# Optimization experiments

Hardware: AMD Instinct MI355X
Metric: run time of the kernel (lower is better)

Reference implementation:

```python
import jax, jax.numpy as jnp
import numpy as np

N, E, D, H, C, L = 100000, 1280000, 64, 4, 16, 3  # nodes, edges, dim, heads, head_dim, layers
NEG_SLOPE = 0.2
LN_EPS = 1e-5


def setup_inputs() -> dict:
    key = jax.random.key(0)
    ks = jax.random.split(key, 6)
    scale = 1.0 / np.sqrt(D)
    x = jax.random.normal(ks[0], (N, D), dtype=jnp.float32)
    edge_index = jax.random.randint(ks[1], (2, E), 0, N, dtype=jnp.int64)
    Wl = jax.random.normal(ks[2], (L, D, H * C), dtype=jnp.float32) * scale  # lin_l (source)
    Wr = jax.random.normal(ks[3], (L, D, H * C), dtype=jnp.float32) * scale  # lin_r (target)
    att = jax.random.normal(ks[4], (L, H, C), dtype=jnp.float32) * scale
    bias = jnp.zeros((L, H * C), dtype=jnp.float32)
    gamma = jnp.ones((L, D), dtype=jnp.float32)
    beta = jnp.zeros((L, D), dtype=jnp.float32)
    return dict(x=x, edge_index=edge_index, Wl=Wl, Wr=Wr, att=att, bias=bias, gamma=gamma, beta=beta)


def _gatv2_conv(x, src, dst, Wl, Wr, att, bias):
    # GATv2Conv (concat=True, share_weights=False, negative_slope=0.2)
    n = x.shape[0]
    xl = (x @ Wl).reshape(n, H, C)  # messages from source nodes
    xr = (x @ Wr).reshape(n, H, C)  # target-side transform
    m = xl[src] + xr[dst]  # [E', H, C]
    e = jnp.einsum('ehc,hc->eh', jax.nn.leaky_relu(m, NEG_SLOPE), att)  # [E', H]
    emax = jax.ops.segment_max(e, dst, num_segments=n)
    p = jnp.exp(e - emax[dst])
    denom = jax.ops.segment_sum(p, dst, num_segments=n)
    alpha = p / denom[dst]  # self-loops guarantee denom > 0
    out = jax.ops.segment_sum(alpha[:, :, None] * xl[src], dst, num_segments=n)  # [N, H, C]
    return out.reshape(n, H * C) + bias


def _layernorm(x, gamma, beta):
    mu = jnp.mean(x, axis=-1, keepdims=True)
    var = jnp.mean(jnp.square(x - mu), axis=-1, keepdims=True)
    return (x - mu) * jax.lax.rsqrt(var + LN_EPS) * gamma + beta


def reference(x, edge_index, Wl, Wr, att, bias, gamma, beta):
    n = x.shape[0]
    loops = jnp.arange(n, dtype=edge_index.dtype)
    src = jnp.concatenate([edge_index[0], loops])  # PyG add_self_loops=True
    dst = jnp.concatenate([edge_index[1], loops])
    for i in range(L):
        x_res = x
        x = _gatv2_conv(x, src, dst, Wl[i], Wr[i], att[i], bias[i])
        x = x + x_res  # residual
        x = _layernorm(x, gamma[i], beta[i])
        x = jax.nn.gelu(x, approximate=False)
    return x
```

## Files before the change

### kernel.cpp

```cpp
#include <hip/hip_runtime.h>
#include <math.h>


#define SCAN_CHUNK 1024

typedef __attribute__((ext_vector_type(8))) short short8;
typedef __attribute__((ext_vector_type(4))) float f32x4;

static inline int cdiv(int a, int b) { return (a + b - 1) / b; }

__device__ __forceinline__ unsigned short bf16_rtn(float v) {
    unsigned u = __float_as_uint(v);
    return (unsigned short)((u + 0x7fffu + ((u >> 16) & 1u)) >> 16);
}


__global__ void csr_init(const unsigned int* __restrict__ ei, int* __restrict__ flag,
                         int* __restrict__ deg, int N) {
    int i = blockIdx.x * blockDim.x + threadIdx.x;
    if (i < N) deg[i] = 1;
    if (blockIdx.x == 0 && threadIdx.x < 64) {
        int nz = (ei[2 * threadIdx.x + 1] != 0u) ? 1 : 0;
        unsigned long long b = __ballot(nz);
        if (threadIdx.x == 0) *flag = (b == 0ull) ? 1 : 0;
    }
}

__global__ void hist_kernel(const int* __restrict__ ei, int E, const int* __restrict__ flag,
                            int* __restrict__ deg, int* __restrict__ pos) {
    int e = blockIdx.x * blockDim.x + threadIdx.x;
    if (e >= E) return;
    int is64 = *flag;
    int d = is64 ? ei[2 * (E + e)] : ei[E + e];
    pos[e] = atomicAdd(&deg[d], 1);
}

__global__ void scan_blocks(const int* __restrict__ deg, int* __restrict__ rowptr,
                            int* __restrict__ partials, int N) {
    __shared__ int sdata[256];
    int t = threadIdx.x;
    int idx0 = blockIdx.x * SCAN_CHUNK + t * 4;
    int v[4]; int sum = 0;
    #pragma unroll
    for (int i = 0; i < 4; ++i) {
        int ii = idx0 + i;
        v[i] = (ii < N) ? deg[ii] : 0;
        sum += v[i];
    }
    sdata[t] = sum;
    __syncthreads();
    for (int off = 1; off < 256; off <<= 1) {
        int val = 0;
        if (t >= off) val = sdata[t - off];
        __syncthreads();
        if (t >= off) sdata[t] += val;
        __syncthreads();
    }
    int run = (t > 0) ? sdata[t - 1] : 0;
    #pragma unroll
    for (int i = 0; i < 4; ++i) {
        int ii = idx0 + i;
        if (ii < N) rowptr[ii] = run;
        run += v[i];
    }
    if (t == 255) partials[blockIdx.x] = sdata[255];
}

__global__ void scan_partials_k(int* __restrict__ partials, int NB) {
    __shared__ int sd[256];
    int t = threadIdx.x;
    sd[t] = (t < NB) ? partials[t] : 0;
    __syncthreads();
    for (int off = 1; off < 256; off <<= 1) {
        int val = 0;
        if (t >= off) val = sd[t - off];
        __syncthreads();
        if (t >= off) sd[t] += val;
        __syncthreads();
    }
    if (t < NB) partials[t] = (t > 0) ? sd[t - 1] : 0;
}

__global__ void add_offsets(int* __restrict__ rowptr, const int* __restrict__ partials,
                            int N, int Etot) {
    int i = blockIdx.x * blockDim.x + threadIdx.x;
    if (i < N) rowptr[i] += partials[i / SCAN_CHUNK];
    if (i == 0) rowptr[N] = Etot;
}

__global__ void fill_csr(const int* __restrict__ ei, int E, int N, const int* __restrict__ flag,
                         const int* __restrict__ rowptr, const int* __restrict__ pos,
                         int* __restrict__ col) {
    int i = blockIdx.x * blockDim.x + threadIdx.x;
    if (i >= E + N) return;
    if (i < E) {
        int is64 = *flag;
        int s = is64 ? ei[2 * i] : ei[i];
        int d = is64 ? ei[2 * (E + i)] : ei[E + i];
        col[rowptr[d] + pos[i]] = s;
    } else {
        int nn = i - E;
        col[rowptr[nn]] = nn;
    }
}

__global__ void wprep_kernel(const float* __restrict__ Wl, const float* __restrict__ Wr,
                             unsigned short* __restrict__ Bh, int Lnum) {
    int t = blockIdx.x * blockDim.x + threadIdx.x;
    int total = Lnum * 2 * 4 * 2 * 64 * 8;
    if (t >= total) return;
    int j    = t & 7;
    int lane = (t >> 3) & 63;
    int kc   = (t >> 9) & 1;
    int ct   = (t >> 10) & 3;
    int h    = (t >> 12) & 1;
    int l    = t >> 13;
    const float* W = (h ? Wr : Wl) + (size_t)l * 4096;
    int k = kc * 32 + (lane >> 4) * 8 + j;
    int c = ct * 16 + (lane & 15);
    Bh[t] = bf16_rtn(W[k * 64 + c]);
}

__global__ __launch_bounds__(256) void transform_mfma(
    const float* __restrict__ x, const unsigned short* __restrict__ Bh,
    float* __restrict__ XL, float* __restrict__ XR, int N) {
    int lane = threadIdx.x & 63;
    int wid = (blockIdx.x * blockDim.x + threadIdx.x) >> 6;
    int nw = (gridDim.x * blockDim.x) >> 6;

    const short8* Bh8 = (const short8*)Bh;
    short8 bh[8][2];
    #pragma unroll
    for (int ct = 0; ct < 8; ++ct)
        #pragma unroll
        for (int kc = 0; kc < 2; ++kc)
            bh[ct][kc] = Bh8[(ct * 2 + kc) * 64 + lane];

    int r16 = lane & 15, kq = lane >> 4;
    int ngroups = N >> 4;

    for (int gidx = wid; gidx < ngroups; gidx += nw) {
        int n0 = gidx << 4;
        const float4* row = (const float4*)(x + (size_t)(n0 + r16) * 64);
        float4 f0 = row[2 * kq], f1 = row[2 * kq + 1];
        float4 f2 = row[8 + 2 * kq], f3 = row[8 + 2 * kq + 1];
        float fa[8] = {f0.x, f0.y, f0.z, f0.w, f1.x, f1.y, f1.z, f1.w};
        float fb[8] = {f2.x, f2.y, f2.z, f2.w, f3.x, f3.y, f3.z, f3.w};
        short8 ah0, ah1, al0, al1;
        #pragma unroll
        for (int j = 0; j < 8; ++j) {
            unsigned short h0 = bf16_rtn(fa[j]);
            unsigned short h1 = bf16_rtn(fb[j]);
            ah0[j] = (short)h0;
            ah1[j] = (short)h1;
            al0[j] = (short)bf16_rtn(fa[j] - __uint_as_float((unsigned)h0 << 16));
            al1[j] = (short)bf16_rtn(fb[j] - __uint_as_float((unsigned)h1 << 16));
        }

        f32x4 acc[8] = {};
        #pragma unroll
        for (int ct = 0; ct < 8; ++ct) {
            acc[ct] = __builtin_amdgcn_mfma_f32_16x16x32_bf16(ah0, bh[ct][0], acc[ct], 0, 0, 0);
            acc[ct] = __builtin_amdgcn_mfma_f32_16x16x32_bf16(ah1, bh[ct][1], acc[ct], 0, 0, 0);
            acc[ct] = __builtin_amdgcn_mfma_f32_16x16x32_bf16(al0, bh[ct][0], acc[ct], 0, 0, 0);
            acc[ct] = __builtin_amdgcn_mfma_f32_16x16x32_bf16(al1, bh[ct][1], acc[ct], 0, 0, 0);
        }
        #pragma unroll
        for (int ct = 0; ct < 4; ++ct)
            #pragma unroll
            for (int r = 0; r < 4; ++r)
                XL[(size_t)(n0 + kq * 4 + r) * 64 + ct * 16 + r16] = acc[ct][r];
        #pragma unroll
        for (int ct = 4; ct < 8; ++ct)
            #pragma unroll
            for (int r = 0; r < 4; ++r)
                XR[(size_t)(n0 + kq * 4 + r) * 64 + (ct - 4) * 16 + r16] = acc[ct][r];
    }
}

__global__ __launch_bounds__(512) void gat_gather_kernel(
    const float* __restrict__ XL, const float* __restrict__ XR,
    const float* __restrict__ x_res,
    const int* __restrict__ rowptr, const int* __restrict__ col,
    const float* __restrict__ att, const float* __restrict__ bias,
    const float* __restrict__ gamma, const float* __restrict__ beta,
    float* __restrict__ x_out, int N) {
    int wid = (blockIdx.x * blockDim.x + threadIdx.x) >> 6;
    if (wid >= N) return;
    int lane = threadIdx.x & 63;
    int g = lane >> 4;
    int c = lane & 15;
    const int n = wid;

    float4 xr = ((const float4*)(XR + (size_t)n * 64))[c];
    float4 av = ((const float4*)att)[c];
    int start = rowptr[n], end = rowptr[n + 1];
    const float4* XL4 = (const float4*)XL;

    float s = 0.f;
    float o0 = 0.f, o1 = 0.f, o2 = 0.f, o3 = 0.f;

    for (int k0 = start; k0 < end; k0 += 8) {
        int ka = k0 + g;
        int kb = ka + 4;
        int sa = col[ka < end ? ka : end - 1];
        int sb = col[kb < end ? kb : end - 1];
        float4 va = XL4[(size_t)sa * 16 + c];
        float4 vb = XL4[(size_t)sb * 16 + c];
        float ta0 = va.x + xr.x; ta0 = fmaxf(ta0, 0.2f * ta0);
        float ta1 = va.y + xr.y; ta1 = fmaxf(ta1, 0.2f * ta1);
        float ta2 = va.z + xr.z; ta2 = fmaxf(ta2, 0.2f * ta2);
        float ta3 = va.w + xr.w; ta3 = fmaxf(ta3, 0.2f * ta3);
        float tb0 = vb.x + xr.x; tb0 = fmaxf(tb0, 0.2f * tb0);
        float tb1 = vb.y + xr.y; tb1 = fmaxf(tb1, 0.2f * tb1);
        float tb2 = vb.z + xr.z; tb2 = fmaxf(tb2, 0.2f * tb2);
        float tb3 = vb.w + xr.w; tb3 = fmaxf(tb3, 0.2f * tb3);
        float wa = ta0 * av.x;
        wa = fmaf(ta1, av.y, wa);
        wa = fmaf(ta2, av.z, wa);
        wa = fmaf(ta3, av.w, wa);
        float wb = tb0 * av.x;
        wb = fmaf(tb1, av.y, wb);
        wb = fmaf(tb2, av.z, wb);
        wb = fmaf(tb3, av.w, wb);
        wa += __shfl_xor(wa, 1);
        wa += __shfl_xor(wa, 2);
        wb += __shfl_xor(wb, 1);
        wb += __shfl_xor(wb, 2);
        wa = (ka < end) ? wa : -1e30f;
        wb = (kb < end) ? wb : -1e30f;
        float pa = __expf(wa);
        float pb = __expf(wb);
        s += pa + pb;
        o0 = fmaf(pa, va.x, o0); o0 = fmaf(pb, vb.x, o0);
        o1 = fmaf(pa, va.y, o1); o1 = fmaf(pb, vb.y, o1);
        o2 = fmaf(pa, va.z, o2); o2 = fmaf(pb, vb.z, o2);
        o3 = fmaf(pa, va.w, o3); o3 = fmaf(pb, vb.w, o3);
    }

    #pragma unroll
    for (int mask = 16; mask <= 32; mask <<= 1) {
        s  += __shfl_xor(s, mask);
        o0 += __shfl_xor(o0, mask);
        o1 += __shfl_xor(o1, mask);
        o2 += __shfl_xor(o2, mask);
        o3 += __shfl_xor(o3, mask);
    }

    float inv = 1.f / s;
    float4 bi = ((const float4*)bias)[c];
    float4 rs = ((const float4*)(x_res + (size_t)n * 64))[c];
    float g0 = fmaf(o0, inv, bi.x + rs.x);
    float g1 = fmaf(o1, inv, bi.y + rs.y);
    float g2 = fmaf(o2, inv, bi.z + rs.z);
    float g3 = fmaf(o3, inv, bi.w + rs.w);

    float loc = g0 + g1 + g2 + g3;
    #pragma unroll
    for (int mask = 1; mask < 16; mask <<= 1) loc += __shfl_xor(loc, mask);
    float mu = loc * (1.f / 64.f);
    float d0 = g0 - mu, d1 = g1 - mu, d2 = g2 - mu, d3 = g3 - mu;
    float vs = d0 * d0 + d1 * d1 + d2 * d2 + d3 * d3;
    #pragma unroll
    for (int mask = 1; mask < 16; mask <<= 1) vs += __shfl_xor(vs, mask);
    float rstd = rsqrtf(vs * (1.f / 64.f) + 1e-5f);
    float4 ga = ((const float4*)gamma)[c];
    float4 be = ((const float4*)beta)[c];
    float y0 = fmaf(d0 * rstd, ga.x, be.x);
    float y1 = fmaf(d1 * rstd, ga.y, be.y);
    float y2 = fmaf(d2 * rstd, ga.z, be.z);
    float y3 = fmaf(d3 * rstd, ga.w, be.w);

    const float k = 0.70710678118654752f;
    float z0 = 0.5f * y0 * (1.f + erff(y0 * k));
    float z1 = 0.5f * y1 * (1.f + erff(y1 * k));
    float z2 = 0.5f * y2 * (1.f + erff(y2 * k));
    float z3 = 0.5f * y3 * (1.f + erff(y3 * k));

    if (g == 0) {
        ((float4*)(x_out + (size_t)n * 64))[c] = make_float4(z0, z1, z2, z3);
    }
}


extern "C" void kernel_launch(void* const* d_in, const int* in_sizes, int n_in,
                              void* d_out, int out_size, void* d_ws, size_t ws_size,
                              hipStream_t stream) {
    const float* x0    = (const float*)d_in[0];
    const int*   ei    = (const int*)d_in[1];
    const float* Wl    = (const float*)d_in[2];
    const float* Wr    = (const float*)d_in[3];
    const float* att   = (const float*)d_in[4];
    const float* bias  = (const float*)d_in[5];
    const float* gamma = (const float*)d_in[6];
    const float* beta  = (const float*)d_in[7];
    float* out = (float*)d_out;

    const int N = in_sizes[0] / 64;
    const int E = in_sizes[1] / 2;
    const int Lnum = in_sizes[2] / (64 * 64);
    const int Etot = E + N;

    char* ws = (char*)d_ws;
    size_t off = 0;
    auto alloc = [&](size_t bytes) {
        void* p = ws + off;
        off = (off + bytes + 255) & ~(size_t)255;
        return p;
    };
    float* XLf    = (float*)alloc((size_t)N * 64 * 4);
    float* XR     = (float*)alloc((size_t)N * 64 * 4);
    float* XA     = (float*)alloc((size_t)N * 64 * 4);
    unsigned short* Bh = (unsigned short*)alloc((size_t)Lnum * 8192 * 2);
    int* rowptr   = (int*)alloc((size_t)(N + 1) * 4);
    int* deg      = (int*)alloc((size_t)N * 4);
    int* pos      = (int*)alloc((size_t)E * 4);
    int* partials = (int*)alloc(1024 * 4);
    int* flag     = (int*)alloc(256);
    int* col      = (int*)alloc((size_t)Etot * 4);

    wprep_kernel<<<cdiv(Lnum * 8192, 256), 256, 0, stream>>>(Wl, Wr, Bh, Lnum);
    csr_init<<<cdiv(N, 256), 256, 0, stream>>>((const unsigned int*)ei, flag, deg, N);
    hist_kernel<<<cdiv(E, 256), 256, 0, stream>>>(ei, E, flag, deg, pos);
    int NB = cdiv(N, SCAN_CHUNK);
    scan_blocks<<<NB, 256, 0, stream>>>(deg, rowptr, partials, N);
    scan_partials_k<<<1, 256, 0, stream>>>(partials, NB);
    add_offsets<<<cdiv(N + 1, 256), 256, 0, stream>>>(rowptr, partials, N, Etot);
    fill_csr<<<cdiv(Etot, 256), 256, 0, stream>>>(ei, E, N, flag, rowptr, pos, col);

    const float* xcur = x0;
    for (int l = 0; l < Lnum; ++l) {
        transform_mfma<<<1600, 256, 0, stream>>>(
            xcur, Bh + (size_t)l * 8192, XLf, XR, N);
        float* xnext = (l == Lnum - 1) ? out : XA;
        gat_gather_kernel<<<cdiv(N * 64, 512), 512, 0, stream>>>(
            XLf, XR, xcur, rowptr, col,
            att + (size_t)l * 64, bias + (size_t)l * 64,
            gamma + (size_t)l * 64, beta + (size_t)l * 64,
            xnext, N);
        xcur = xnext;
    }
}
```

Measured before the change: 423.7 us.

## Stage transform outputs through LDS and simplify gather indexing and epilogue

The MFMA transform now writes its accumulator tiles into a padded per-wave shared-memory buffer and then stores whole float4 rows, so XL/XR writes are coalesced instead of scattered 4-byte stores. The transform grid shrinks from 1600 to 512 blocks. The gather kernel drops the per-edge index clamp by padding col with 8 trailing zeros, and uses 32-bit index math. The LayerNorm/GELU epilogue is rewritten to one element per lane with full-wave reductions and a full 64-lane store, so no lanes are left idle. The trade-offs are extra LDS traffic and shuffles, and correctness depends on out-of-range edges still being masked later in the loop.

Measured after the change: 409.5 us. 1.03x faster.

```diff
diff --git a/kernel.cpp b/kernel.cpp
--- a/kernel.cpp
+++ b/kernel.cpp
@@ -92,7 +92,9 @@
                          const int* __restrict__ rowptr, const int* __restrict__ pos,
                          int* __restrict__ col) {
     int i = blockIdx.x * blockDim.x + threadIdx.x;
-    if (i >= E + N) return;
+    int Etot = E + N;
+    if (i >= Etot + 8) return;
+    if (i >= Etot) { col[Etot + (i - Etot)] = 0; return; }
     if (i < E) {
         int is64 = *flag;
         int s = is64 ? ei[2 * i] : ei[i];
@@ -124,7 +126,9 @@
 __global__ __launch_bounds__(256) void transform_mfma(
     const float* __restrict__ x, const unsigned short* __restrict__ Bh,
     float* __restrict__ XL, float* __restrict__ XR, int N) {
+    __shared__ float stage[4][16 * 68];
     int lane = threadIdx.x & 63;
+    int wv = threadIdx.x >> 6;
     int wid = (blockIdx.x * blockDim.x + threadIdx.x) >> 6;
     int nw = (gridDim.x * blockDim.x) >> 6;
 
@@ -138,6 +142,7 @@
 
     int r16 = lane & 15, kq = lane >> 4;
     int ngroups = N >> 4;
+    float* sbuf = stage[wv];
 
     for (int gidx = wid; gidx < ngroups; gidx += nw) {
         int n0 = gidx << 4;
@@ -166,15 +171,20 @@
             acc[ct] = __builtin_amdgcn_mfma_f32_16x16x32_bf16(al1, bh[ct][1], acc[ct], 0, 0, 0);
         }
         #pragma unroll
-        for (int ct = 0; ct < 4; ++ct)
+        for (int half = 0; half < 2; ++half) {
             #pragma unroll
-            for (int r = 0; r < 4; ++r)
-                XL[(size_t)(n0 + kq * 4 + r) * 64 + ct * 16 + r16] = acc[ct][r];
-        #pragma unroll
-        for (int ct = 4; ct < 8; ++ct)
+            for (int ct = 0; ct < 4; ++ct)
+                #pragma unroll
+                for (int r = 0; r < 4; ++r)
+                    sbuf[(kq * 4 + r) * 68 + ct * 16 + r16] = acc[half * 4 + ct][r];
+            float4* dst4 = (float4*)((half ? XR : XL) + (size_t)n0 * 64);
             #pragma unroll
-            for (int r = 0; r < 4; ++r)
-                XR[(size_t)(n0 + kq * 4 + r) * 64 + (ct - 4) * 16 + r16] = acc[ct][r];
+            for (int w = 0; w < 4; ++w) {
+                int rr = w * 4 + kq;
+                float4 v = ((const float4*)sbuf)[rr * 17 + r16];
+                dst4[rr * 16 + r16] = v;
+            }
+        }
     }
 }
 
@@ -203,10 +213,10 @@
     for (int k0 = start; k0 < end; k0 += 8) {
         int ka = k0 + g;
         int kb = ka + 4;
-        int sa = col[ka < end ? ka : end - 1];
-        int sb = col[kb < end ? kb : end - 1];
-        float4 va = XL4[(size_t)sa * 16 + c];
-        float4 vb = XL4[(size_t)sb * 16 + c];
+        int sa = col[ka];
+        int sb = col[kb];
+        float4 va = XL4[sa * 16 + c];
+        float4 vb = XL4[sb * 16 + c];
         float ta0 = va.x + xr.x; ta0 = fmaxf(ta0, 0.2f * ta0);
         float ta1 = va.y + xr.y; ta1 = fmaxf(ta1, 0.2f * ta1);
         float ta2 = va.z + xr.z; ta2 = fmaxf(ta2, 0.2f * ta2);
@@ -247,39 +257,30 @@
         o3 += __shfl_xor(o3, mask);
     }
 
-    float inv = 1.f / s;
-    float4 bi = ((const float4*)bias)[c];
-    float4 rs = ((const float4*)(x_res + (size_t)n * 64))[c];
-    float g0 = fmaf(o0, inv, bi.x + rs.x);
-    float g1 = fmaf(o1, inv, bi.y + rs.y);
-    float g2 = fmaf(o2, inv, bi.z + rs.z);
-    float g3 = fmaf(o3, inv, bi.w + rs.w);
-
-    float loc = g0 + g1 + g2 + g3;
-    #pragma unroll
-    for (int mask = 1; mask < 16; mask <<= 1) loc += __shfl_xor(loc, mask);
-    float mu = loc * (1.f / 64.f);
-    float d0 = g0 - mu, d1 = g1 - mu, d2 = g2 - mu, d3 = g3 - mu;
-    float vs = d0 * d0 + d1 * d1 + d2 * d2 + d3 * d3;
-    #pragma unroll
-    for (int mask = 1; mask < 16; mask <<= 1) vs += __shfl_xor(vs, mask);
+    int srcLane = lane >> 2;
+    int j = lane & 3;
+    float o0t = __shfl(o0, srcLane);
+    float o1t = __shfl(o1, srcLane);
+    float o2t = __shfl(o2, srcLane);
+    float o3t = __shfl(o3, srcLane);
+    float st  = __shfl(s,  srcLane);
+    float ov = (j & 2) ? ((j & 1) ? o3t : o2t) : ((j & 1) ? o1t : o0t);
+
+    float gval = ov / st + bias[lane] + x_res[(size_t)n * 64 + lane];
+
+    float mu = gval;
+    #pragma unroll
+    for (int mask = 1; mask < 64; mask <<= 1) mu += __shfl_xor(mu, mask);
+    mu *= (1.f / 64.f);
+    float d = gval - mu;
+    float vs = d * d;
+    #pragma unroll
+    for (int mask = 1; mask < 64; mask <<= 1) vs += __shfl_xor(vs, mask);
     float rstd = rsqrtf(vs * (1.f / 64.f) + 1e-5f);
-    float4 ga = ((const float4*)gamma)[c];
-    float4 be = ((const float4*)beta)[c];
-    float y0 = fmaf(d0 * rstd, ga.x, be.x);
-    float y1 = fmaf(d1 * rstd, ga.y, be.y);
-    float y2 = fmaf(d2 * rstd, ga.z, be.z);
-    float y3 = fmaf(d3 * rstd, ga.w, be.w);
-
-    const float k = 0.70710678118654752f;
-    float z0 = 0.5f * y0 * (1.f + erff(y0 * k));
-    float z1 = 0.5f * y1 * (1.f + erff(y1 * k));
-    float z2 = 0.5f * y2 * (1.f + erff(y2 * k));
-    float z3 = 0.5f * y3 * (1.f + erff(y3 * k));
-
-    if (g == 0) {
-        ((float4*)(x_out + (size_t)n * 64))[c] = make_float4(z0, z1, z2, z3);
-    }
+    float y = fmaf(d * rstd, gamma[lane], beta[lane]);
+
+    float z = 0.5f * y * (1.f + erff(y * 0.70710678118654752f));
+    x_out[(size_t)n * 64 + lane] = z;
 }
 
 
@@ -317,7 +318,7 @@
     int* pos      = (int*)alloc((size_t)E * 4);
     int* partials = (int*)alloc(1024 * 4);
     int* flag     = (int*)alloc(256);
-    int* col      = (int*)alloc((size_t)Etot * 4);
+    int* col      = (int*)alloc((size_t)(Etot + 8) * 4);
 
     wprep_kernel<<<cdiv(Lnum * 8192, 256), 256, 0, stream>>>(Wl, Wr, Bh, Lnum);
     csr_init<<<cdiv(N, 256), 256, 0, stream>>>((const unsigned int*)ei, flag, deg, N);
@@ -326,11 +327,11 @@
     scan_blocks<<<NB, 256, 0, stream>>>(deg, rowptr, partials, N);
     scan_partials_k<<<1, 256, 0, stream>>>(partials, NB);
     add_offsets<<<cdiv(N + 1, 256), 256, 0, stream>>>(rowptr, partials, N, Etot);
-    fill_csr<<<cdiv(Etot, 256), 256, 0, stream>>>(ei, E, N, flag, rowptr, pos, col);
+    fill_csr<<<cdiv(Etot + 8, 256), 256, 0, stream>>>(ei, E, N, flag, rowptr, pos, col);
 
     const float* xcur = x0;
     for (int l = 0; l < Lnum; ++l) {
-        transform_mfma<<<1600, 256, 0, stream>>>(
+        transform_mfma<<<512, 256, 0, stream>>>(
             xcur, Bh + (size_t)l * 8192, XLf, XR, N);
         float* xnext = (l == Lnum - 1) ? out : XA;
         gat_gather_kernel<<<cdiv(N * 64, 512), 512, 0, stream>>>(
```
